# Kernel optimization log

Hardware: AMD Instinct MI355X
Metric: run time of the kernel (lower is better)

Reference implementation:

```python
import jax, jax.numpy as jnp
import numpy as np

EMBED_DIM = 1024
NUM_HEADS = 16
MICRO_HEADS = 8
HEAD_DIM = EMBED_DIM // NUM_HEADS
N_BLOCKS = NUM_HEADS // MICRO_HEADS
B, N = 2, 2048


def setup_inputs() -> dict:
    key = jax.random.key(0)
    ks = jax.random.split(key, 9)
    s = 1.0 / np.sqrt(EMBED_DIM)
    return {
        "x": jax.random.normal(ks[0], (B, N, EMBED_DIM), dtype=jnp.float32),
        "Wq": jax.random.uniform(ks[1], (EMBED_DIM, EMBED_DIM), jnp.float32, -s, s),
        "bq": jax.random.uniform(ks[2], (EMBED_DIM,), jnp.float32, -s, s),
        "Wk": jax.random.uniform(ks[3], (EMBED_DIM, EMBED_DIM), jnp.float32, -s, s),
        "bk": jax.random.uniform(ks[4], (EMBED_DIM,), jnp.float32, -s, s),
        "Wv": jax.random.uniform(ks[5], (EMBED_DIM, EMBED_DIM), jnp.float32, -s, s),
        "bv": jax.random.uniform(ks[6], (EMBED_DIM,), jnp.float32, -s, s),
        "Wo": jax.random.uniform(ks[7], (EMBED_DIM, EMBED_DIM), jnp.float32, -s, s),
        "bo": jax.random.uniform(ks[8], (EMBED_DIM,), jnp.float32, -s, s),
    }


def _scramble(t, b, n):
    # Replicates torch's Qh[:, :, hs:he, :].contiguous().view(B*mh, N, dh)
    # which is a raw row-major reshape mixing (N, mh) -> (mh, N) per batch.
    # (B, N, E) -> (B, N, nb, mh, dh) -> (B, nb, N, mh, dh) -> raw reshape -> (B, nb, mh, N, dh)
    t = t.reshape(b, n, N_BLOCKS, MICRO_HEADS, HEAD_DIM)
    t = jnp.transpose(t, (0, 2, 1, 3, 4))
    return t.reshape(b, N_BLOCKS, MICRO_HEADS, n, HEAD_DIM)


def reference(x, Wq, bq, Wk, bk, Wv, bv, Wo, bo):
    b, n, e = x.shape
    scale = HEAD_DIM ** -0.5
    Q = x @ Wq.T + bq
    K = x @ Wk.T + bk
    V = x @ Wv.T + bv
    q = _scramble(Q, b, n)  # (B, nb, mh, N, dh)
    k = _scramble(K, b, n)
    v = _scramble(V, b, n)
    s = jnp.einsum("bgmqd,bgmkd->bgmqk", q, k) * scale  # (B, nb, mh, N, N)
    causal = jnp.tril(jnp.ones((n, n), dtype=bool))
    s = jnp.where(causal, s, -jnp.inf)
    p = jax.nn.softmax(s, axis=-1)
    ctx = jnp.einsum("bgmqk,bgmkd->bgmqd", p, v)  # (B, nb, mh, N, dh)
    # inverse raw reshape: (mh, N, dh) -> (N, mh*dh) per (b, g), then concat blocks
    ctx = ctx.reshape(b, N_BLOCKS, n, MICRO_HEADS * HEAD_DIM)
    ctx = jnp.transpose(ctx, (0, 2, 1, 3)).reshape(b, n, e)
    return ctx @ Wo.T + bo
```

## Files before the change

kernel.cpp:

```cpp
#include <hip/hip_runtime.h>
#include <hip/hip_bf16.h>

typedef unsigned short ushortT;
typedef __attribute__((ext_vector_type(8))) short short8;
typedef __attribute__((ext_vector_type(4))) float floatx4;
typedef __attribute__((ext_vector_type(2))) unsigned int uintx2;

__device__ inline ushortT f2bf(float f) {
    union { float f; unsigned int i; } v; v.f = f;
    unsigned int x = v.i;
    return (ushortT)((x + 0x7fffu + ((x >> 16) & 1u)) >> 16);
}

__device__ inline void gl_lds16(const ushortT* g, ushortT* lds) {
    __builtin_amdgcn_global_load_lds(
        (const __attribute__((address_space(1))) unsigned int*)g,
        (__attribute__((address_space(3))) unsigned int*)lds, 16, 0, 0);
}

__global__ __launch_bounds__(256) void cvt_bf16(
    const float* __restrict__ x,
    const float* __restrict__ Wq, const float* __restrict__ Wk,
    const float* __restrict__ Wv, const float* __restrict__ Wo,
    ushortT* __restrict__ xb, ushortT* __restrict__ Wb)
{
    const unsigned tid = blockIdx.x * 256 + threadIdx.x;
    const size_t e = (size_t)tid * 8;
    const float* src;
    ushortT* dst;
    size_t off;
    if (e < (size_t)(4u << 20)) { src = x; dst = xb; off = e; }
    else {
        const size_t r = e - (size_t)(4u << 20);
        const int wsel = (int)(r >> 20);
        off = r & 0xFFFFFu;
        src = (wsel == 0) ? Wq : (wsel == 1) ? Wk : (wsel == 2) ? Wv : Wo;
        dst = Wb + ((size_t)wsel << 20);
    }
    const float4 f0 = ((const float4*)(src + off))[0];
    const float4 f1 = ((const float4*)(src + off))[1];
    union { __hip_bfloat162 h[4]; uint4 u; } pk;
    pk.h[0] = __float22bfloat162_rn(float2{f0.x, f0.y});
    pk.h[1] = __float22bfloat162_rn(float2{f0.z, f0.w});
    pk.h[2] = __float22bfloat162_rn(float2{f1.x, f1.y});
    pk.h[3] = __float22bfloat162_rn(float2{f1.z, f1.w});
    *(uint4*)(dst + off) = pk.u;
}

__global__ __launch_bounds__(512, 2) void gemm_qkv_8p(
    const ushortT* __restrict__ A, const ushortT* __restrict__ Wst,
    const float* __restrict__ b0, const float* __restrict__ b1, const float* __restrict__ b2,
    ushortT* __restrict__ O0, ushortT* __restrict__ O1, ushortT* __restrict__ VT)
{
    __shared__ __align__(16) ushortT sm[65536];

    const int t = threadIdx.x;
    const int bid = blockIdx.x;
    const int wg = (bid & 7) * 24 + (bid >> 3);
    const int mt = wg / 12;
    const int nt = wg - mt * 12;
    const int m0 = mt * 256;
    const int mat = nt >> 2;
    const int n0 = (nt & 3) * 256;
    const ushortT* W = Wst + ((size_t)mat << 20);
    const float* bias = (mat == 0) ? b0 : (mat == 1) ? b1 : b2;
    ushortT* Out     = (mat == 0) ? O0 : O1;
    const float oscale = (mat == 0) ? 0.18033688f : 1.0f;

    const int w = t >> 6, lane = t & 63;
    const int wm = w >> 2, wn = w & 3;
    const int col16 = lane & 15, quad = lane >> 4;
    const int c7 = col16 & 7;

    const int ko[2] = { ((0 + quad) ^ c7) << 3, ((4 + quad) ^ c7) << 3 };
    const int xbase = (wm * 128 + col16) * 64;
    const int wbase = (wn * 64 + col16) * 64;

    const int trow = t >> 3;
    const int sch = (t & 7) ^ (trow & 7);
    const ushortT* gA[4]; const ushortT* gB[4];
    #pragma unroll
    for (int q = 0; q < 4; q++) {
        gA[q] = A + (size_t)(m0 + q * 64 + trow) * 1024 + sch * 8;
        gB[q] = W + (size_t)(n0 + q * 64 + trow) * 1024 + sch * 8;
    }
    const int dst0 = (w << 6) * 8;

    floatx4 acc[8][4];
    #pragma unroll
    for (int i = 0; i < 8; i++)
        #pragma unroll
        for (int j = 0; j < 4; j++) acc[i][j] = (floatx4)0.0f;

    auto issue8 = [&](const int ab, const int bb) {
        #pragma unroll
        for (int q = 0; q < 4; q++) {
            gl_lds16(gA[q], sm + ab + dst0 + q * 4096);
            gl_lds16(gB[q], sm + bb + dst0 + q * 4096);
            gA[q] += 64; gB[q] += 64;
        }
    };

    auto group = [&](const int ab, const int bb) {
        short8 bw[4];
        #pragma unroll
        for (int ks = 0; ks < 2; ks++) {
            #pragma unroll
            for (int mh = 0; mh < 2; mh++) {
                short8 bx[4];
                if (mh == 0) {
                    #pragma unroll
                    for (int nf = 0; nf < 4; nf++)
                        bw[nf] = *(const short8*)(sm + bb + wbase + nf * 1024 + ko[ks]);
                }
                #pragma unroll
                for (int j = 0; j < 4; j++)
                    bx[j] = *(const short8*)(sm + ab + xbase + (mh * 4 + j) * 1024 + ko[ks]);
                __builtin_amdgcn_s_barrier();
                __builtin_amdgcn_s_setprio(1);
                #pragma unroll
                for (int j = 0; j < 4; j++)
                    #pragma unroll
                    for (int nf = 0; nf < 4; nf++)
                        acc[mh * 4 + j][nf] = __builtin_amdgcn_mfma_f32_16x16x32_bf16(
                            bw[nf], bx[j], acc[mh * 4 + j][nf], 0, 0, 0);
                __builtin_amdgcn_s_setprio(0);
                __builtin_amdgcn_s_barrier();
            }
        }
    };

    issue8(0, 16384);
    issue8(32768, 49152);

    #pragma unroll 1
    for (int it = 0; it < 7; ++it) {
        asm volatile("s_waitcnt vmcnt(8)" ::: "memory");
        __builtin_amdgcn_s_barrier();
        group(0, 16384);
        issue8(0, 16384);
        asm volatile("s_waitcnt vmcnt(8)" ::: "memory");
        __builtin_amdgcn_s_barrier();
        group(32768, 49152);
        issue8(32768, 49152);
    }
    asm volatile("s_waitcnt vmcnt(8)" ::: "memory");
    __builtin_amdgcn_s_barrier();
    group(0, 16384);
    asm volatile("s_waitcnt vmcnt(0)" ::: "memory");
    __builtin_amdgcn_s_barrier();
    group(32768, 49152);

    if (mat != 2) {
        #pragma unroll
        for (int mf = 0; mf < 8; mf++) {
            const int m = m0 + wm * 128 + mf * 16 + col16;
            #pragma unroll
            for (int nf = 0; nf < 4; nf++) {
                const int nb = n0 + wn * 64 + nf * 16 + quad * 4;
                const float4 bv4 = *(const float4*)(bias + nb);
                const float v0 = (acc[mf][nf][0] + bv4.x) * oscale;
                const float v1 = (acc[mf][nf][1] + bv4.y) * oscale;
                const float v2 = (acc[mf][nf][2] + bv4.z) * oscale;
                const float v3 = (acc[mf][nf][3] + bv4.w) * oscale;
                union { __hip_bfloat162 h[2]; unsigned long long u; } pk2;
                pk2.h[0] = __float22bfloat162_rn(float2{v0, v1});
                pk2.h[1] = __float22bfloat162_rn(float2{v2, v3});
                *(unsigned long long*)(Out + (size_t)m * 1024 + nb) = pk2.u;
            }
        }
    } else {
        __syncthreads();
        #pragma unroll
        for (int mf = 0; mf < 8; mf++) {
            const int ml = wm * 128 + mf * 16 + col16;
            const int pib = ml * 4 + wn;
            #pragma unroll
            for (int nf = 0; nf < 4; nf++) {
                const int dbase = nf * 16 + quad * 4;
                const float4 bv4 = *(const float4*)(bias + n0 + wn * 64 + dbase);
                sm[(dbase + 0) * 1024 + pib] = f2bf(acc[mf][nf][0] + bv4.x);
                sm[(dbase + 1) * 1024 + pib] = f2bf(acc[mf][nf][1] + bv4.y);
                sm[(dbase + 2) * 1024 + pib] = f2bf(acc[mf][nf][2] + bv4.z);
                sm[(dbase + 3) * 1024 + pib] = f2bf(acc[mf][nf][3] + bv4.w);
            }
        }
        __syncthreads();
        const int b2 = mt >> 3, mhh = mt & 7, gg = n0 >> 9;
        const int p0 = (n0 & 511) >> 6;
        ushortT* vbase = VT + (size_t)((b2 * 2 + gg) * 8 + mhh) * 131072 + p0;
        #pragma unroll
        for (int v = 0; v < 32; v++) {
            const int e = v * 512 + t;
            const int d = e >> 8;
            const int runml = e & 255;
            const uint2 val = *(const uint2*)(sm + d * 1024 + runml * 4);
            *(uint2*)(vbase + d * 2048 + runml * 8) = val;
        }
    }
}

template <bool OUT_F32, bool N64>
__global__ __launch_bounds__(256) void gemm_lds(
    const ushortT* __restrict__ A, const ushortT* __restrict__ Wst,
    const float* __restrict__ b0, const float* __restrict__ b1, const float* __restrict__ b2,
    void* __restrict__ O0, void* __restrict__ O1, void* __restrict__ O2)
{
    constexpr int NT = N64 ? 64 : 128;
    constexpr int NJ = N64 ? 2 : 4;
    constexpr int WQ = N64 ? 2 : 4;
    __shared__ __align__(16) ushortT As[128 * 64];
    __shared__ __align__(16) ushortT Bs[NT * 64];
    const int t = threadIdx.x;
    const int m0 = blockIdx.y * 128;
    const int n0g = blockIdx.x * NT;
    const int mat = n0g >> 10;
    const int n0 = n0g & 1023;
    const ushortT* W = Wst + ((size_t)mat << 20);
    const float* bias = (mat == 0) ? b0 : (mat == 1) ? b1 : b2;
    void* Out        = (mat == 0) ? O0 : (mat == 1) ? O1 : O2;

    const int w = t >> 6, lane = t & 63;
    const int wm = w >> 1, wn = w & 1;
    const int col16 = lane & 15, quad = lane >> 4;

    floatx4 acc[4][NJ];
    for (int i = 0; i < 4; i++)
        for (int j = 0; j < NJ; j++) acc[i][j] = (floatx4)0.0f;

    const int cid0 = w * (N64 ? 128 : 256) + lane;

    for (int k0 = 0; k0 < 1024; k0 += 64) {
        #pragma unroll
        for (int q = 0; q < 4; q++) {
            const int cid = w * 256 + q * 64 + lane;
            const int row = cid >> 3;
            const int sch = (cid & 7) ^ (row & 7);
            gl_lds16(A + (size_t)(m0 + row) * 1024 + k0 + sch * 8,
                     As + (size_t)(w * 256 + q * 64) * 8);
        }
        #pragma unroll
        for (int q = 0; q < WQ; q++) {
            const int cid = cid0 + q * 64;
            const int row = cid >> 3;
            const int sch = (cid & 7) ^ (row & 7);
            gl_lds16(W + (size_t)(n0 + row) * 1024 + k0 + sch * 8,
                     Bs + (size_t)(w * (N64 ? 128 : 256) + q * 64) * 8);
        }
        __syncthreads();
        #pragma unroll
        for (int ks = 0; ks < 64; ks += 32) {
            const int cbase = (ks >> 3) + quad;
            const int sw = col16 & 7;
            short8 a[4], b[NJ];
            #pragma unroll
            for (int i = 0; i < 4; i++) {
                const int row = wm * 64 + i * 16 + col16;
                a[i] = *(const short8*)(As + row * 64 + ((cbase ^ sw) << 3));
            }
            #pragma unroll
            for (int j = 0; j < NJ; j++) {
                const int row = wn * (NT / 2) + j * 16 + col16;
                b[j] = *(const short8*)(Bs + row * 64 + ((cbase ^ sw) << 3));
            }
            #pragma unroll
            for (int i = 0; i < 4; i++)
                #pragma unroll
                for (int j = 0; j < NJ; j++)
                    acc[i][j] = __builtin_amdgcn_mfma_f32_16x16x32_bf16(b[j], a[i], acc[i][j], 0, 0, 0);
        }
        __syncthreads();
    }

    #pragma unroll
    for (int i = 0; i < 4; i++) {
        const int m = m0 + wm * 64 + i * 16 + col16;
        #pragma unroll
        for (int j = 0; j < NJ; j++) {
            const int nb = n0 + wn * (NT / 2) + j * 16 + quad * 4;
            const float4 bv4 = *(const float4*)(bias + nb);
            const float v0 = acc[i][j][0] + bv4.x;
            const float v1 = acc[i][j][1] + bv4.y;
            const float v2 = acc[i][j][2] + bv4.z;
            const float v3 = acc[i][j][3] + bv4.w;
            if constexpr (OUT_F32) {
                *(float4*)((float*)Out + (size_t)m * 1024 + nb) = float4{v0, v1, v2, v3};
            } else {
                union { __hip_bfloat162 h[2]; unsigned long long u; } pk2;
                pk2.h[0] = __float22bfloat162_rn(float2{v0, v1});
                pk2.h[1] = __float22bfloat162_rn(float2{v2, v3});
                *(unsigned long long*)((ushortT*)Out + (size_t)m * 1024 + nb) = pk2.u;
            }
        }
    }
}

__global__ __launch_bounds__(512, 4) void attn(
    const ushortT* __restrict__ Qb, const ushortT* __restrict__ Kb,
    const ushortT* __restrict__ VT, ushortT* __restrict__ Cb)
{
    __shared__ __align__(16) ushortT lds[16384];

    const int t = threadIdx.x;
    const int bid = blockIdx.x;
    const int xcd = bid & 7;
    const int u = bid >> 3;
    const int s = xcd * 4 + (u & 3);
    const int x4 = u >> 2;
    const int p = (x4 < 8) ? x4 : 23 - x4;
    const int bb = s >> 4, g = (s >> 3) & 1, mh = s & 7;

    const int w = t >> 6, lane = t & 63;
    const int col16 = lane & 15, quad = lane >> 4;

    const size_t baseoff = (size_t)bb * 2048 * 1024 + (size_t)g * 512;
    const size_t vtbase  = (size_t)s * 64 * 2048;
    const int i0 = mh * 2048 + p * 128;
    const int ntile = 2 * p + 2;
    const int qloc = w * 16 + col16;
    const int c7 = col16 & 7;

    short8 qreg[2];
    {
        const int i = i0 + qloc;
        const ushortT* ptr = Qb + baseoff + (size_t)(i >> 3) * 1024 + (i & 7) * 64;
        qreg[0] = *(const short8*)(ptr + quad * 8);
        qreg[1] = *(const short8*)(ptr + 32 + quad * 8);
    }

    int kbo[2];
    kbo[0] = col16 * 64 + (((0 + quad) ^ c7) << 3);
    kbo[1] = col16 * 64 + (((4 + quad) ^ c7) << 3);

    const int row = t >> 3;
    const int sch = (t & 7) ^ (row & 7);
    const int jr = mh * 2048 + row;
    const ushortT* gk = Kb + baseoff + (size_t)(jr >> 3) * 1024 + (jr & 7) * 64 + sch * 8;
    const ushortT* gv = VT + vtbase + (size_t)row * 2048 + sch * 8;
    const int sdK = w * 512;

    auto stage = [&](int sb) {
        gl_lds16(gk, lds + sb + sdK);
        gl_lds16(gv, lds + sb + 8192 + sdK);
        gk += 8192; gv += 64;
    };

    float l4[4] = {0.f, 0.f, 0.f, 0.f};
    floatx4 Oacc[4];
    for (int c = 0; c < 4; c++) Oacc[c] = (floatx4)0.0f;

    stage(0);
    int sb = 4096;
    #pragma unroll 1
    for (int kt = 0; kt < ntile; ++kt) {
        __syncthreads();
        if (kt < ntile - 1) { stage(sb); sb ^= 4096; }

        floatx4 sc[4];
        for (int c = 0; c < 4; c++) sc[c] = (floatx4)0.0f;
        #pragma unroll
        for (int h = 0; h < 2; h++) {
            const short8 bq = qreg[h];
            #pragma unroll
            for (int c = 0; c < 4; c++) {
                const short8 ak = *(const short8*)(lds + kbo[h] + c * 1024);
                sc[c] = __builtin_amdgcn_mfma_f32_16x16x32_bf16(ak, bq, sc[c], 0, 0, 0);
            }
        }

        const int dk = kt - 2 * p;
        if (dk >= 0) {
            const int qe = qloc - 64 * dk;
            #pragma unroll
            for (int c = 0; c < 4; c++)
                #pragma unroll
                for (int r = 0; r < 4; r++)
                    if ((c * 16 + quad * 4 + r) > qe) sc[c][r] = -1e30f;
        }

        unsigned pw[4][2];
        #pragma unroll
        for (int c = 0; c < 4; c++) {
            float pv0 = __builtin_amdgcn_exp2f(sc[c][0]);
            float pv1 = __builtin_amdgcn_exp2f(sc[c][1]);
            float pv2 = __builtin_amdgcn_exp2f(sc[c][2]);
            float pv3 = __builtin_amdgcn_exp2f(sc[c][3]);
            l4[0] += pv0; l4[1] += pv1; l4[2] += pv2; l4[3] += pv3;
            union { __hip_bfloat162 h; unsigned u; } a, b;
            a.h = __float22bfloat162_rn(float2{pv0, pv1});
            b.h = __float22bfloat162_rn(float2{pv2, pv3});
            pw[c][0] = a.u; pw[c][1] = b.u;
        }

        #pragma unroll
        for (int h = 0; h < 2; h++) {
            unsigned dw[4];
            #pragma unroll
            for (int uu = 0; uu < 2; uu++) {
                uintx2 s32 = __builtin_amdgcn_permlane32_swap(pw[2 * h][uu], pw[2 * h + 1][uu], false, false);
                uintx2 s16 = __builtin_amdgcn_permlane16_swap(s32.x, s32.y, false, false);
                dw[uu] = s16.x; dw[2 + uu] = s16.y;
            }
            union { unsigned u2[4]; short8 s2; } bpu;
            bpu.u2[0] = dw[0]; bpu.u2[1] = dw[1]; bpu.u2[2] = dw[2]; bpu.u2[3] = dw[3];
            const short8 bp = bpu.s2;
            #pragma unroll
            for (int c = 0; c < 4; c++) {
                const short8 av = *(const short8*)(lds + kbo[h] + 8192 + c * 1024);
                Oacc[c] = __builtin_amdgcn_mfma_f32_16x16x32_bf16(av, bp, Oacc[c], 0, 0, 0);
            }
        }

        kbo[0] ^= 4096; kbo[1] ^= 4096;
    }

    float l_s = (l4[0] + l4[1]) + (l4[2] + l4[3]);
    l_s += __shfl_xor(l_s, 16);
    l_s += __shfl_xor(l_s, 32);

    {
        const int i = i0 + qloc;
        const float inv = 1.0f / l_s;
        ushortT* dst = Cb + baseoff + (size_t)(i >> 3) * 1024 + (i & 7) * 64;
        #pragma unroll
        for (int c = 0; c < 4; c++) {
            union { __hip_bfloat162 h[2]; unsigned long long u2; } pk2;
            pk2.h[0] = __float22bfloat162_rn(float2{Oacc[c][0] * inv, Oacc[c][1] * inv});
            pk2.h[1] = __float22bfloat162_rn(float2{Oacc[c][2] * inv, Oacc[c][3] * inv});
            *(unsigned long long*)(dst + c * 16 + quad * 4) = pk2.u2;
        }
    }
}

extern "C" void kernel_launch(void* const* d_in, const int* in_sizes, int n_in,
                              void* d_out, int out_size, void* d_ws, size_t ws_size,
                              hipStream_t stream)
{
    const float* x  = (const float*)d_in[0];
    const float* Wq = (const float*)d_in[1];
    const float* bq = (const float*)d_in[2];
    const float* Wk = (const float*)d_in[3];
    const float* bk = (const float*)d_in[4];
    const float* Wv = (const float*)d_in[5];
    const float* bv = (const float*)d_in[6];
    const float* Wo = (const float*)d_in[7];
    const float* bo = (const float*)d_in[8];

    const size_t M1 = (size_t)1024 * 1024;
    ushortT* Wb  = (ushortT*)d_ws;
    ushortT* xb  = Wb + 4 * M1;
    ushortT* Qb  = xb + 4 * M1;
    ushortT* Kb  = Qb + 4 * M1;
    ushortT* VTb = Wb + 16 * M1;
    ushortT* Cb  = Qb;

    dim3 blk(256);
    cvt_bf16<<<dim3(4096), blk, 0, stream>>>(x, Wq, Wk, Wv, Wo, xb, Wb);
    gemm_qkv_8p<<<dim3(192), dim3(512), 0, stream>>>(
        xb, Wb, bq, bk, bv, Qb, Kb, VTb);
    attn<<<dim3(512), dim3(512), 0, stream>>>(Qb, Kb, VTb, Cb);
    gemm_lds<true, true><<<dim3(16, 32), blk, 0, stream>>>(
        Cb, Wb + 3 * M1, bo, bo, bo, d_out, d_out, d_out);
}
```

Before: 177.1 us.

## Switch attention to 32x32 MFMA with split-key wave pairs and LDS reduction

Reworks the attention inner loop to use 32x32x16 bf16 MFMA instead of 16x16x32. Each pair of waves shares a 32-query group and splits the 64 keys of a tile between them, then merges partial outputs and row sums through LDS at the end. It also adds s_setprio around MFMA bursts and drops one cross-lane shuffle stage. The intent is fewer LDS reads per FLOP and fewer permlane operations. In exchange it adds a larger LDS buffer, an extra end-of-kernel reduction with two barriers, and half of the waves sit idle during the final store.

```diff
diff --git a/kernel.cpp b/kernel.cpp
--- a/kernel.cpp
+++ b/kernel.cpp
@@ -4,6 +4,7 @@
 typedef unsigned short ushortT;
 typedef __attribute__((ext_vector_type(8))) short short8;
 typedef __attribute__((ext_vector_type(4))) float floatx4;
+typedef __attribute__((ext_vector_type(16))) float floatx16;
 typedef __attribute__((ext_vector_type(2))) unsigned int uintx2;
 
 __device__ inline ushortT f2bf(float f) {
@@ -299,7 +300,7 @@
     const ushortT* __restrict__ Qb, const ushortT* __restrict__ Kb,
     const ushortT* __restrict__ VT, ushortT* __restrict__ Cb)
 {
-    __shared__ __align__(16) ushortT lds[16384];
+    __shared__ __align__(16) ushortT lds[20480];
 
     const int t = threadIdx.x;
     const int bid = blockIdx.x;
@@ -311,26 +312,30 @@
     const int bb = s >> 4, g = (s >> 3) & 1, mh = s & 7;
 
     const int w = t >> 6, lane = t & 63;
-    const int col16 = lane & 15, quad = lane >> 4;
+    const int l31 = lane & 31, h = lane >> 5;
+    const int qgrp = w >> 1, kh = w & 1;
 
     const size_t baseoff = (size_t)bb * 2048 * 1024 + (size_t)g * 512;
     const size_t vtbase  = (size_t)s * 64 * 2048;
     const int i0 = mh * 2048 + p * 128;
     const int ntile = 2 * p + 2;
-    const int qloc = w * 16 + col16;
-    const int c7 = col16 & 7;
-
-    short8 qreg[2];
+    const int qloc = qgrp * 32 + l31;
+
+    short8 qreg[4];
     {
         const int i = i0 + qloc;
         const ushortT* ptr = Qb + baseoff + (size_t)(i >> 3) * 1024 + (i & 7) * 64;
-        qreg[0] = *(const short8*)(ptr + quad * 8);
-        qreg[1] = *(const short8*)(ptr + 32 + quad * 8);
-    }
-
-    int kbo[2];
-    kbo[0] = col16 * 64 + (((0 + quad) ^ c7) << 3);
-    kbo[1] = col16 * 64 + (((4 + quad) ^ c7) << 3);
+        #pragma unroll
+        for (int dc = 0; dc < 4; dc++)
+            qreg[dc] = *(const short8*)(ptr + dc * 16 + h * 8);
+    }
+
+    int off[2][4];
+    #pragma unroll
+    for (int a = 0; a < 2; a++)
+        #pragma unroll
+        for (int b = 0; b < 4; b++)
+            off[a][b] = (a * 32 + l31) * 64 + ((((b << 1) + h) ^ (lane & 7)) << 3);
 
     const int row = t >> 3;
     const int sch = (t & 7) ^ (row & 7);
@@ -346,89 +351,103 @@
     };
 
     float l4[4] = {0.f, 0.f, 0.f, 0.f};
-    floatx4 Oacc[4];
-    for (int c = 0; c < 4; c++) Oacc[c] = (floatx4)0.0f;
+    floatx16 Oacc[2];
+    Oacc[0] = (floatx16)0.0f; Oacc[1] = (floatx16)0.0f;
 
     stage(0);
     int sb = 4096;
+    int sbR = 0;
     #pragma unroll 1
     for (int kt = 0; kt < ntile; ++kt) {
         __syncthreads();
         if (kt < ntile - 1) { stage(sb); sb ^= 4096; }
 
-        floatx4 sc[4];
-        for (int c = 0; c < 4; c++) sc[c] = (floatx4)0.0f;
-        #pragma unroll
-        for (int h = 0; h < 2; h++) {
-            const short8 bq = qreg[h];
-            #pragma unroll
-            for (int c = 0; c < 4; c++) {
-                const short8 ak = *(const short8*)(lds + kbo[h] + c * 1024);
-                sc[c] = __builtin_amdgcn_mfma_f32_16x16x32_bf16(ak, bq, sc[c], 0, 0, 0);
-            }
-        }
+        floatx16 sc = (floatx16)0.0f;
+        __builtin_amdgcn_s_setprio(1);
+        #pragma unroll
+        for (int dc = 0; dc < 4; dc++) {
+            const short8 ak = *(const short8*)(lds + sbR + off[kh][dc]);
+            sc = __builtin_amdgcn_mfma_f32_32x32x16_bf16(ak, qreg[dc], sc, 0, 0, 0);
+        }
+        __builtin_amdgcn_s_setprio(0);
 
         const int dk = kt - 2 * p;
         if (dk >= 0) {
             const int qe = qloc - 64 * dk;
             #pragma unroll
-            for (int c = 0; c < 4; c++)
-                #pragma unroll
-                for (int r = 0; r < 4; r++)
-                    if ((c * 16 + quad * 4 + r) > qe) sc[c][r] = -1e30f;
-        }
-
-        unsigned pw[4][2];
-        #pragma unroll
-        for (int c = 0; c < 4; c++) {
-            float pv0 = __builtin_amdgcn_exp2f(sc[c][0]);
-            float pv1 = __builtin_amdgcn_exp2f(sc[c][1]);
-            float pv2 = __builtin_amdgcn_exp2f(sc[c][2]);
-            float pv3 = __builtin_amdgcn_exp2f(sc[c][3]);
-            l4[0] += pv0; l4[1] += pv1; l4[2] += pv2; l4[3] += pv3;
-            union { __hip_bfloat162 h; unsigned u; } a, b;
-            a.h = __float22bfloat162_rn(float2{pv0, pv1});
-            b.h = __float22bfloat162_rn(float2{pv2, pv3});
-            pw[c][0] = a.u; pw[c][1] = b.u;
-        }
-
-        #pragma unroll
-        for (int h = 0; h < 2; h++) {
-            unsigned dw[4];
-            #pragma unroll
-            for (int uu = 0; uu < 2; uu++) {
-                uintx2 s32 = __builtin_amdgcn_permlane32_swap(pw[2 * h][uu], pw[2 * h + 1][uu], false, false);
-                uintx2 s16 = __builtin_amdgcn_permlane16_swap(s32.x, s32.y, false, false);
-                dw[uu] = s16.x; dw[2 + uu] = s16.y;
-            }
-            union { unsigned u2[4]; short8 s2; } bpu;
-            bpu.u2[0] = dw[0]; bpu.u2[1] = dw[1]; bpu.u2[2] = dw[2]; bpu.u2[3] = dw[3];
-            const short8 bp = bpu.s2;
-            #pragma unroll
-            for (int c = 0; c < 4; c++) {
-                const short8 av = *(const short8*)(lds + kbo[h] + 8192 + c * 1024);
-                Oacc[c] = __builtin_amdgcn_mfma_f32_16x16x32_bf16(av, bp, Oacc[c], 0, 0, 0);
-            }
-        }
-
-        kbo[0] ^= 4096; kbo[1] ^= 4096;
+            for (int r = 0; r < 16; r++) {
+                const int key = kh * 32 + (r & 3) + ((r >> 2) << 3) + 4 * h;
+                if (key > qe) sc[r] = -1e30f;
+            }
+        }
+
+        unsigned sp[8];
+        #pragma unroll
+        for (int i2 = 0; i2 < 8; i2++) {
+            const float p0 = __builtin_amdgcn_exp2f(sc[2 * i2]);
+            const float p1 = __builtin_amdgcn_exp2f(sc[2 * i2 + 1]);
+            l4[(2 * i2) & 3] += p0;
+            l4[(2 * i2 + 1) & 3] += p1;
+            union { __hip_bfloat162 hh; unsigned uu; } pk;
+            pk.hh = __float22bfloat162_rn(float2{p0, p1});
+            sp[i2] = pk.uu;
+        }
+
+        #pragma unroll
+        for (int kc = 0; kc < 2; kc++) {
+            const uintx2 s0 = __builtin_amdgcn_permlane32_swap(
+                sp[4 * kc + 0], sp[4 * kc + 2], false, false);
+            const uintx2 s1 = __builtin_amdgcn_permlane32_swap(
+                sp[4 * kc + 1], sp[4 * kc + 3], false, false);
+            union { unsigned uu[4]; short8 ss; } bp;
+            bp.uu[0] = s0.x; bp.uu[1] = s1.x; bp.uu[2] = s0.y; bp.uu[3] = s1.y;
+            const int kcg = kh * 2 + kc;
+            __builtin_amdgcn_s_setprio(1);
+            #pragma unroll
+            for (int dt = 0; dt < 2; dt++) {
+                const short8 av = *(const short8*)(lds + sbR + 8192 + off[dt][kcg]);
+                Oacc[dt] = __builtin_amdgcn_mfma_f32_32x32x16_bf16(av, bp.ss, Oacc[dt], 0, 0, 0);
+            }
+            __builtin_amdgcn_s_setprio(0);
+        }
+
+        sbR ^= 4096;
     }
 
     float l_s = (l4[0] + l4[1]) + (l4[2] + l4[3]);
-    l_s += __shfl_xor(l_s, 16);
     l_s += __shfl_xor(l_s, 32);
 
-    {
+    __syncthreads();
+    float* cb = (float*)lds;
+    const int ci = (qgrp * 64 + lane) * 33;
+    if (kh == 1) {
+        #pragma unroll
+        for (int dt = 0; dt < 2; dt++)
+            #pragma unroll
+            for (int r = 0; r < 16; r++) cb[ci + dt * 16 + r] = Oacc[dt][r];
+        cb[ci + 32] = l_s;
+    }
+    __syncthreads();
+    if (kh == 0) {
+        #pragma unroll
+        for (int dt = 0; dt < 2; dt++)
+            #pragma unroll
+            for (int r = 0; r < 16; r++) Oacc[dt][r] += cb[ci + dt * 16 + r];
+        l_s += cb[ci + 32];
+        const float inv = 1.0f / l_s;
         const int i = i0 + qloc;
-        const float inv = 1.0f / l_s;
         ushortT* dst = Cb + baseoff + (size_t)(i >> 3) * 1024 + (i & 7) * 64;
         #pragma unroll
-        for (int c = 0; c < 4; c++) {
-            union { __hip_bfloat162 h[2]; unsigned long long u2; } pk2;
-            pk2.h[0] = __float22bfloat162_rn(float2{Oacc[c][0] * inv, Oacc[c][1] * inv});
-            pk2.h[1] = __float22bfloat162_rn(float2{Oacc[c][2] * inv, Oacc[c][3] * inv});
-            *(unsigned long long*)(dst + c * 16 + quad * 4) = pk2.u2;
-        }
+        for (int dt = 0; dt < 2; dt++)
+            #pragma unroll
+            for (int rq = 0; rq < 4; rq++) {
+                union { __hip_bfloat162 hh[2]; unsigned long long uu; } pk2;
+                pk2.hh[0] = __float22bfloat162_rn(
+                    float2{Oacc[dt][4 * rq + 0] * inv, Oacc[dt][4 * rq + 1] * inv});
+                pk2.hh[1] = __float22bfloat162_rn(
+                    float2{Oacc[dt][4 * rq + 2] * inv, Oacc[dt][4 * rq + 3] * inv});
+                *(unsigned long long*)(dst + dt * 32 + 8 * rq + 4 * h) = pk2.uu;
+            }
     }
 }
 
```

Result: slower. 195.7 us (+10.5%).
